# Kernel tuning notes

Hardware: AMD Instinct MI355X
Metric: run time of the kernel (lower is better)

## Reference

```python
import jax, jax.numpy as jnp
import numpy as np

N_NODES = 50000
N_EDGES = 800000
EPS = 1e-16

def _gat_layer(x, row, col, W, a_src, a_dst, b, heads, concat):
    N = x.shape[0]
    C = a_src.shape[1]
    h = (x @ W).reshape(N, heads, C)                       # [N,H,C]
    al_src = jnp.sum(h * a_src, axis=-1)                    # [N,H]
    al_dst = jnp.sum(h * a_dst, axis=-1)                    # [N,H]
    e = jax.nn.leaky_relu(al_src[row] + al_dst[col], 0.2)   # [E,H]
    # segment softmax over destination node (col)
    m = jax.ops.segment_max(e, col, num_segments=N)
    e = jnp.exp(e - m[col])
    s = jax.ops.segment_sum(e, col, num_segments=N)
    alpha = e / (s[col] + EPS)                              # [E,H]
    msg = h[row] * alpha[:, :, None]                        # [E,H,C]
    out = jax.ops.segment_sum(msg, col, num_segments=N)     # [N,H,C]
    out = out.reshape(N, heads * C) if concat else out.mean(axis=1)
    return out + b

def setup_inputs() -> dict:
    key = jax.random.key(0)
    ks = jax.random.split(key, 16)
    d_in, hid, d_out, d_edge, H = 64, 64, 32, 16, 4
    inp = {
        "x": jax.random.normal(ks[0], (N_NODES, d_in), jnp.float32),
        "edge_index": jax.random.randint(ks[1], (2, N_EDGES), 0, N_NODES, jnp.int32),
        "edge_attr": jax.random.normal(ks[2], (N_EDGES, d_edge), jnp.float32),
        "W1": jax.random.normal(ks[3], (d_in, H * hid), jnp.float32) * 0.1,
        "a1_src": jax.random.normal(ks[4], (H, hid), jnp.float32) * 0.1,
        "a1_dst": jax.random.normal(ks[5], (H, hid), jnp.float32) * 0.1,
        "b1": jax.random.normal(ks[6], (H * hid,), jnp.float32) * 0.1,
        "W2": jax.random.normal(ks[7], (H * hid, hid), jnp.float32) * 0.05,
        "a2_src": jax.random.normal(ks[8], (1, hid), jnp.float32) * 0.1,
        "a2_dst": jax.random.normal(ks[9], (1, hid), jnp.float32) * 0.1,
        "b2": jax.random.normal(ks[10], (hid,), jnp.float32) * 0.1,
        "Wn": jax.random.normal(ks[11], (hid, d_out), jnp.float32) * 0.1,
        "bn": jax.random.normal(ks[12], (d_out,), jnp.float32) * 0.1,
        "We": jax.random.normal(ks[13], (2 * hid + d_edge, 1), jnp.float32) * 0.1,
        "be": jax.random.normal(ks[14], (1,), jnp.float32) * 0.1,
    }
    return inp

def reference(x, edge_index, edge_attr, W1, a1_src, a1_dst, b1, W2, a2_src, a2_dst, b2, Wn, bn, We, be):
    N = x.shape[0]
    row0, col0 = edge_index[0], edge_index[1]
    # PyG GATConv default: add self loops for message passing
    loops = jnp.arange(N, dtype=edge_index.dtype)
    row = jnp.concatenate([row0, loops])
    col = jnp.concatenate([col0, loops])
    h = jax.nn.elu(_gat_layer(x, row, col, W1, a1_src, a1_dst, b1, heads=4, concat=True))
    h = jax.nn.elu(_gat_layer(h, row, col, W2, a2_src, a2_dst, b2, heads=1, concat=False))
    node_out = h @ Wn + bn                                   # [N, out]
    edge_feat = jnp.concatenate([h[row0], h[col0], edge_attr], axis=1)  # [E, 2*hid+d_edge]
    edge_out = edge_feat @ We + be                           # [E, 1]
    return (node_out, edge_out)
```

## Files before the change

kernel.cpp:

```cpp
#include <hip/hip_runtime.h>
#include <hip/hip_bf16.h>

#define N_NODES 50000
#define N_EDGES 800000
#define N_TOT   850000
#define MAXD    128

#define NBUCK 196
#define BCAP  8192

typedef __hip_bfloat16 bf16;
typedef __attribute__((ext_vector_type(8))) short bf16x8;
typedef __attribute__((ext_vector_type(4))) float f32x4;

__device__ __forceinline__ unsigned short f2bu(float v){
  union { bf16 b; unsigned short u; } cv; cv.b = __float2bfloat16(v); return cv.u;
}
__device__ __forceinline__ float bflo(unsigned int d){ return __uint_as_float(d << 16); }
__device__ __forceinline__ float bfhi(unsigned int d){ return __uint_as_float(d & 0xffff0000u); }

__global__ __launch_bounds__(256) void initb_kernel(int* __restrict__ bcur){
  int i = threadIdx.x;
  if (i < NBUCK) bcur[i] = i * BCAP;
}

__global__ __launch_bounds__(256) void binscatter_kernel(const int* __restrict__ ei,
    int* __restrict__ bcur, unsigned int* __restrict__ pairbuf){
  __shared__ int hist[NBUCK];
  __shared__ int gbase[NBUCK];
  int tid = threadIdx.x;
  if (tid < NBUCK) hist[tid] = 0;
  __syncthreads();
  int base = blockIdx.x * 4096;
  #pragma unroll 4
  for (int i = 0; i < 16; ++i) {
    int k = base + i*256 + tid;
    if (k < N_TOT) {
      int c = (k < N_EDGES) ? ei[N_EDGES + k] : (k - N_EDGES);
      atomicAdd(&hist[c >> 8], 1);
    }
  }
  __syncthreads();
  if (tid < NBUCK) {
    int h = hist[tid];
    gbase[tid] = h ? atomicAdd(&bcur[tid], h) : 0;
    hist[tid] = 0;
  }
  __syncthreads();
  #pragma unroll 4
  for (int i = 0; i < 16; ++i) {
    int k = base + i*256 + tid;
    if (k < N_TOT) {
      int r, c;
      if (k < N_EDGES) { r = ei[k]; c = ei[N_EDGES + k]; } else { r = c = k - N_EDGES; }
      int b = c >> 8;
      int lpos = atomicAdd(&hist[b], 1);
      pairbuf[gbase[b] + lpos] = (unsigned)r | ((unsigned)(c & 255) << 16);
    }
  }
}

__global__ __launch_bounds__(256) void bcount_kernel(const unsigned int* __restrict__ pairbuf,
    const int* __restrict__ bcur, int* __restrict__ cnt){
  __shared__ int lhist[256];
  int b = blockIdx.x, tid = threadIdx.x;
  lhist[tid] = 0;
  __syncthreads();
  int base = b * BCAP;
  int size = bcur[b] - base; if (size > BCAP) size = BCAP;
  for (int j = tid; j < size; j += 256)
    atomicAdd(&lhist[pairbuf[base + j] >> 16], 1);
  __syncthreads();
  int node = b*256 + tid;
  if (node < N_NODES) cnt[node] = lhist[tid];
}

__global__ __launch_bounds__(1024) void scanA_kernel(const int* __restrict__ cnt, int* __restrict__ psum){
  __shared__ int wsum[16];
  int tid = threadIdx.x, i = blockIdx.x*1024 + tid;
  int v = (i < N_NODES) ? cnt[i] : 0;
  #pragma unroll
  for (int off = 32; off; off >>= 1) v += __shfl_xor(v, off, 64);
  if ((tid & 63) == 0) wsum[tid >> 6] = v;
  __syncthreads();
  if (tid < 64) {
    int t = (tid < 16) ? wsum[tid] : 0;
    #pragma unroll
    for (int off = 8; off; off >>= 1) t += __shfl_xor(t, off, 64);
    if (tid == 0) psum[blockIdx.x] = t;
  }
}

__global__ __launch_bounds__(64) void scanB_kernel(int* __restrict__ psum, int nparts){
  int lane = threadIdx.x;
  int v = (lane < nparts) ? psum[lane] : 0;
  #pragma unroll
  for (int off = 1; off < 64; off <<= 1) {
    int t = __shfl_up(v, off, 64);
    if (lane >= off) v += t;
  }
  int e = __shfl_up(v, 1, 64);
  if (lane == 0) e = 0;
  if (lane < nparts) psum[lane] = e;
}

__global__ __launch_bounds__(1024) void scanC_kernel(const int* __restrict__ cnt, const int* __restrict__ psum,
                                                     int* __restrict__ offs){
  __shared__ int sm[1024];
  int tid = threadIdx.x, b = blockIdx.x, i = b*1024 + tid;
  int v = (i < N_NODES) ? cnt[i] : 0;
  sm[tid] = v;
  __syncthreads();
  for (int off = 1; off < 1024; off <<= 1) {
    int t = (tid >= off) ? sm[tid - off] : 0;
    __syncthreads();
    sm[tid] += t;
    __syncthreads();
  }
  if (i < N_NODES) offs[i] = psum[b] + sm[tid] - v;
  if (b == 0 && tid == 0) offs[N_NODES] = N_TOT;
}

__global__ __launch_bounds__(256) void lscatter_kernel(const unsigned int* __restrict__ pairbuf,
    const int* __restrict__ bcur, const int* __restrict__ offs, int* __restrict__ srcs){
  __shared__ int lcur[256];
  int b = blockIdx.x, tid = threadIdx.x;
  int lo = b*256;
  if (lo + tid < N_NODES) lcur[tid] = offs[lo + tid];
  __syncthreads();
  int base = b * BCAP;
  int size = bcur[b] - base; if (size > BCAP) size = BCAP;
  for (int j = tid; j < size; j += 256) {
    unsigned v = pairbuf[base + j];
    int pos = atomicAdd(&lcur[v >> 16], 1);
    srcs[pos] = (int)(v & 0xFFFFu);
  }
}

__global__ __launch_bounds__(256) void wfrag_kernel(const float* __restrict__ W1, const float* __restrict__ W2,
    const float* __restrict__ a1s, const float* __restrict__ a1d,
    unsigned short* __restrict__ wf1, unsigned short* __restrict__ wf2,
    float* __restrict__ ws1, float* __restrict__ wd1){
  int b = blockIdx.x, tid = threadIdx.x;
  if (b < 128) {
    int i = b*256 + tid;
    if (i < 16384) {
      int k = i >> 8, n = i & 255;
      int kk = k >> 5, qq = (k >> 3) & 3, j = k & 7, nt = n >> 4, cc = n & 15;
      wf1[(((kk*16 + nt)*4 + qq)*16 + cc)*8 + j] = f2bu(W1[i]);
    } else {
      int i2 = i - 16384;
      int k = i2 >> 6, n = i2 & 63;
      int kk = k >> 5, qq = (k >> 3) & 3, j = k & 7, ch = n >> 4, cc = n & 15;
      wf2[(((kk*4 + ch)*4 + qq)*16 + cc)*8 + j] = f2bu(W2[i2]);
    }
  } else {
    int k = tid >> 2, h = tid & 3;
    const float* wrow = W1 + k*256 + h*64;
    const float* as = a1s + h*64;
    const float* ad = a1d + h*64;
    float ss = 0.f, sd = 0.f;
    #pragma unroll 8
    for (int c = 0; c < 64; ++c) {
      float wv = wrow[c];
      ss = fmaf(wv, as[c], ss);
      sd = fmaf(wv, ad[c], sd);
    }
    ws1[k*4 + h] = ss;
    wd1[k*4 + h] = sd;
  }
}

__global__ __launch_bounds__(256) void xprep_kernel(const float* __restrict__ x,
    const float* __restrict__ ws1, const float* __restrict__ wd1,
    unsigned short* __restrict__ xb, float* __restrict__ al1s, float* __restrict__ al1d){
  __shared__ float sws[64][4], swd[64][4];
  int tid = threadIdx.x;
  sws[tid >> 2][tid & 3] = ws1[tid];
  swd[tid >> 2][tid & 3] = wd1[tid];
  __syncthreads();
  int lane = tid & 63, wave = tid >> 6;
  int g = lane & 15, sub = lane >> 4;
  int n = blockIdx.x*16 + wave*4 + sub;
  float4 xv = *(const float4*)(x + (size_t)n*64 + g*4);
  uint2 dd;
  dd.x = (unsigned)f2bu(xv.x) | ((unsigned)f2bu(xv.y) << 16);
  dd.y = (unsigned)f2bu(xv.z) | ((unsigned)f2bu(xv.w) << 16);
  ((uint2*)xb)[(size_t)n*16 + g] = dd;
  int c0 = g*4;
  float ps0 = 0.f, ps1 = 0.f, ps2 = 0.f, ps3 = 0.f;
  float pd0 = 0.f, pd1 = 0.f, pd2 = 0.f, pd3 = 0.f;
  float xc[4] = {xv.x, xv.y, xv.z, xv.w};
  #pragma unroll
  for (int i = 0; i < 4; ++i) {
    int c = c0 + i;
    ps0 = fmaf(xc[i], sws[c][0], ps0); ps1 = fmaf(xc[i], sws[c][1], ps1);
    ps2 = fmaf(xc[i], sws[c][2], ps2); ps3 = fmaf(xc[i], sws[c][3], ps3);
    pd0 = fmaf(xc[i], swd[c][0], pd0); pd1 = fmaf(xc[i], swd[c][1], pd1);
    pd2 = fmaf(xc[i], swd[c][2], pd2); pd3 = fmaf(xc[i], swd[c][3], pd3);
  }
  #pragma unroll
  for (int off = 1; off < 16; off <<= 1) {
    ps0 += __shfl_xor(ps0, off, 64); ps1 += __shfl_xor(ps1, off, 64);
    ps2 += __shfl_xor(ps2, off, 64); ps3 += __shfl_xor(ps3, off, 64);
    pd0 += __shfl_xor(pd0, off, 64); pd1 += __shfl_xor(pd1, off, 64);
    pd2 += __shfl_xor(pd2, off, 64); pd3 += __shfl_xor(pd3, off, 64);
  }
  if (g < 4)      al1s[(size_t)n*4 + g]       = (g==0)?ps0:(g==1)?ps1:(g==2)?ps2:ps3;
  else if (g < 8) al1d[(size_t)n*4 + (g-4)]   = (g==4)?pd0:(g==5)?pd1:(g==6)?pd2:pd3;
}

__global__ __launch_bounds__(256, 8) void attn1x_kernel(const unsigned short* __restrict__ xb,
    const float* __restrict__ al1s, const float* __restrict__ al1d,
    const int* __restrict__ offs, const int* __restrict__ srcs,
    bf16* __restrict__ ag){
  __shared__ __align__(16) float ebuf[4][MAXD+4][4];
  __shared__ int sbuf[4][MAXD+4];

  int wave = threadIdx.x >> 6, lane = threadIdx.x & 63;
  int n = blockIdx.x*4 + wave;
  int start = offs[n], end = offs[n+1];
  int deg = end - start;
  int lim = deg < MAXD ? deg : MAXD;
  float4 aldv = *(const float4*)(al1d + (size_t)n*4);
  float ald0 = aldv.x, ald1 = aldv.y, ald2 = aldv.z, ald3 = aldv.w;

  float s0 = 0.f, s1 = 0.f, s2 = 0.f, s3 = 0.f;
  {
    int idx = lane;
    for (int j = start + lane; j < end; j += 64, idx += 64) {
      int r = srcs[j];
      float4 als = *(const float4*)(al1s + (size_t)r*4);
      float e0 = als.x + ald0; e0 = e0 >= 0.f ? e0 : 0.2f*e0; float p0 = __expf(e0); s0 += p0;
      float e1 = als.y + ald1; e1 = e1 >= 0.f ? e1 : 0.2f*e1; float p1 = __expf(e1); s1 += p1;
      float e2 = als.z + ald2; e2 = e2 >= 0.f ? e2 : 0.2f*e2; float p2 = __expf(e2); s2 += p2;
      float e3 = als.w + ald3; e3 = e3 >= 0.f ? e3 : 0.2f*e3; float p3 = __expf(e3); s3 += p3;
      if (idx < MAXD) {
        sbuf[wave][idx] = r;
        *(float4*)&ebuf[wave][idx][0] = make_float4(p0, p1, p2, p3);
      }
    }
  }
  if (lane < 4) {
    int ip = lim + lane;
    sbuf[wave][ip] = 0;
    *(float4*)&ebuf[wave][ip][0] = make_float4(0.f, 0.f, 0.f, 0.f);
  }
  #pragma unroll
  for (int off = 32; off; off >>= 1) {
    s0 += __shfl_xor(s0, off, 64);
    s1 += __shfl_xor(s1, off, 64);
    s2 += __shfl_xor(s2, off, 64);
    s3 += __shfl_xor(s3, off, 64);
  }
  float inv0 = 1.f/(s0 + 1e-16f), inv1 = 1.f/(s1 + 1e-16f);
  float inv2 = 1.f/(s2 + 1e-16f), inv3 = 1.f/(s3 + 1e-16f);

  int cl = lane & 15, es = lane >> 4;
  float acc[4][4];
  #pragma unroll
  for (int h = 0; h < 4; ++h)
    #pragma unroll
    for (int i = 0; i < 4; ++i) acc[h][i] = 0.f;
  {
    const uint2* base2 = (const uint2*)xb;
    #pragma unroll 2
    for (int jj = 0; jj < lim; jj += 4) {
      int idx = jj + es;
      int r = sbuf[wave][idx];
      float4 pv = *(const float4*)&ebuf[wave][idx][0];
      uint2 d = base2[(size_t)r*16 + cl];
      float c0 = bflo(d.x), c1 = bfhi(d.x), c2 = bflo(d.y), c3 = bfhi(d.y);
      acc[0][0] = fmaf(pv.x, c0, acc[0][0]); acc[0][1] = fmaf(pv.x, c1, acc[0][1]);
      acc[0][2] = fmaf(pv.x, c2, acc[0][2]); acc[0][3] = fmaf(pv.x, c3, acc[0][3]);
      acc[1][0] = fmaf(pv.y, c0, acc[1][0]); acc[1][1] = fmaf(pv.y, c1, acc[1][1]);
      acc[1][2] = fmaf(pv.y, c2, acc[1][2]); acc[1][3] = fmaf(pv.y, c3, acc[1][3]);
      acc[2][0] = fmaf(pv.z, c0, acc[2][0]); acc[2][1] = fmaf(pv.z, c1, acc[2][1]);
      acc[2][2] = fmaf(pv.z, c2, acc[2][2]); acc[2][3] = fmaf(pv.z, c3, acc[2][3]);
      acc[3][0] = fmaf(pv.w, c0, acc[3][0]); acc[3][1] = fmaf(pv.w, c1, acc[3][1]);
      acc[3][2] = fmaf(pv.w, c2, acc[3][2]); acc[3][3] = fmaf(pv.w, c3, acc[3][3]);
    }
  }
  if (deg > MAXD) {
    const uint2* base2 = (const uint2*)xb;
    for (int jj = MAXD; jj < deg; jj += 4) {
      int idx = jj + es;
      bool ok = idx < deg;
      int j = ok ? (start + idx) : start;
      int r = srcs[j];
      float4 als = *(const float4*)(al1s + (size_t)r*4);
      float e0 = als.x + ald0; e0 = e0 >= 0.f ? e0 : 0.2f*e0; float p0 = __expf(e0);
      float e1 = als.y + ald1; e1 = e1 >= 0.f ? e1 : 0.2f*e1; float p1 = __expf(e1);
      float e2 = als.z + ald2; e2 = e2 >= 0.f ? e2 : 0.2f*e2; float p2 = __expf(e2);
      float e3 = als.w + ald3; e3 = e3 >= 0.f ? e3 : 0.2f*e3; float p3 = __expf(e3);
      float m = ok ? 1.f : 0.f;
      uint2 d = base2[(size_t)r*16 + cl];
      float c0 = bflo(d.x)*m, c1 = bfhi(d.x)*m, c2 = bflo(d.y)*m, c3 = bfhi(d.y)*m;
      acc[0][0] = fmaf(p0, c0, acc[0][0]); acc[0][1] = fmaf(p0, c1, acc[0][1]);
      acc[0][2] = fmaf(p0, c2, acc[0][2]); acc[0][3] = fmaf(p0, c3, acc[0][3]);
      acc[1][0] = fmaf(p1, c0, acc[1][0]); acc[1][1] = fmaf(p1, c1, acc[1][1]);
      acc[1][2] = fmaf(p1, c2, acc[1][2]); acc[1][3] = fmaf(p1, c3, acc[1][3]);
      acc[2][0] = fmaf(p2, c0, acc[2][0]); acc[2][1] = fmaf(p2, c1, acc[2][1]);
      acc[2][2] = fmaf(p2, c2, acc[2][2]); acc[2][3] = fmaf(p2, c3, acc[2][3]);
      acc[3][0] = fmaf(p3, c0, acc[3][0]); acc[3][1] = fmaf(p3, c1, acc[3][1]);
      acc[3][2] = fmaf(p3, c2, acc[3][2]); acc[3][3] = fmaf(p3, c3, acc[3][3]);
    }
  }
  #pragma unroll
  for (int h = 0; h < 4; ++h)
    #pragma unroll
    for (int i = 0; i < 4; ++i) {
      acc[h][i] += __shfl_xor(acc[h][i], 16, 64);
      acc[h][i] += __shfl_xor(acc[h][i], 32, 64);
    }
  {
    float invh = (es==0)?inv0:(es==1)?inv1:(es==2)?inv2:inv3;
    float o0 = ((es==0)?acc[0][0]:(es==1)?acc[1][0]:(es==2)?acc[2][0]:acc[3][0]) * invh;
    float o1 = ((es==0)?acc[0][1]:(es==1)?acc[1][1]:(es==2)?acc[2][1]:acc[3][1]) * invh;
    float o2 = ((es==0)?acc[0][2]:(es==1)?acc[1][2]:(es==2)?acc[2][2]:acc[3][2]) * invh;
    float o3 = ((es==0)?acc[0][3]:(es==1)?acc[1][3]:(es==2)?acc[2][3]:acc[3][3]) * invh;
    uint2 dd;
    dd.x = (unsigned)f2bu(o0) | ((unsigned)f2bu(o1) << 16);
    dd.y = (unsigned)f2bu(o2) | ((unsigned)f2bu(o3) << 16);
    ((uint2*)ag)[(size_t)n*64 + lane] = dd;
  }
}

__global__ __launch_bounds__(256) void gemm1b_kernel(const unsigned short* __restrict__ ag,
    const unsigned short* __restrict__ wf1, const float* __restrict__ b1, bf16* __restrict__ h1){
  __shared__ __align__(16) unsigned short ctile[32*264];
  int tid = threadIdx.x, wave = tid >> 6, lane = tid & 63;
  int q = lane >> 4, c = lane & 15;
  int n0 = blockIdx.x * 64;

  union { uint4 u; bf16x8 v; } bfr[2][4];
  #pragma unroll
  for (int kk = 0; kk < 2; ++kk)
    #pragma unroll
    for (int nti = 0; nti < 4; ++nti)
      bfr[kk][nti].u = *(const uint4*)(wf1 + (size_t)((((kk*16 + wave*4 + nti)*4 + q)*16 + c)*8));

  float b1v[4];
  #pragma unroll
  for (int nti = 0; nti < 4; ++nti) b1v[nti] = b1[(wave*4 + nti)*16 + c];

  #pragma unroll
  for (int half = 0; half < 2; ++half) {
    #pragma unroll
    for (int sti = 0; sti < 2; ++sti) {
      int st = half*2 + sti;
      int row = n0 + st*16 + c;
      if (row >= N_NODES) row = N_NODES - 1;
      bf16x8 afr[2];
      #pragma unroll
      for (int kk = 0; kk < 2; ++kk) {
        union { uint4 u; bf16x8 v; } a;
        a.u = *(const uint4*)(ag + (size_t)row*256 + wave*64 + kk*32 + q*8);
        afr[kk] = a.v;
      }
      #pragma unroll
      for (int nti = 0; nti < 4; ++nti) {
        f32x4 acc = {0.f, 0.f, 0.f, 0.f};
        #pragma unroll
        for (int kk = 0; kk < 2; ++kk)
          acc = __builtin_amdgcn_mfma_f32_16x16x32_bf16(afr[kk], bfr[kk][nti].v, acc, 0, 0, 0);
        int lrow = sti*16 + q*4, nt = wave*4 + nti;
        #pragma unroll
        for (int r = 0; r < 4; ++r) {
          float o = acc[r] + b1v[nti];
          o = o > 0.f ? o : expm1f(o);
          ctile[(lrow + r)*264 + nt*16 + c] = f2bu(o);
        }
      }
    }
    __syncthreads();
    #pragma unroll 1
    for (int i = 0; i < 8; ++i) {
      int lr = wave*8 + i;
      int node = n0 + half*32 + lr;
      if (node < N_NODES) {
        uint2 dd = *(const uint2*)&ctile[lr*264 + lane*4];
        ((uint2*)h1)[(size_t)node*64 + lane] = dd;
      }
    }
    __syncthreads();
  }
}

__global__ __launch_bounds__(256) void gemm2_kernel(const bf16* __restrict__ h1, const unsigned short* __restrict__ wf2,
    const float* __restrict__ a2s, const float* __restrict__ a2d,
    bf16* __restrict__ h2pre, float* __restrict__ al2s, float* __restrict__ al2d){
  __shared__ __align__(16) float ctile[64][65];
  int tid = threadIdx.x, wave = tid >> 6, lane = tid & 63;
  int q = lane >> 4, c = lane & 15;
  int n0 = blockIdx.x * 64;

  union { uint4 u; bf16x8 v; } bfr[8];
  #pragma unroll
  for (int kk = 0; kk < 8; ++kk)
    bfr[kk].u = *(const uint4*)(wf2 + (size_t)((((kk*4 + wave)*4 + q)*16 + c)*8));

  const unsigned short* h1u = (const unsigned short*)h1;
  #pragma unroll 1
  for (int st = 0; st < 4; ++st) {
    if (n0 + st*16 >= N_NODES) break;
    f32x4 acc = {0.f, 0.f, 0.f, 0.f};
    size_t arow = (size_t)(n0 + st*16 + c)*256 + q*8;
    #pragma unroll
    for (int kk = 0; kk < 8; ++kk) {
      union { uint4 u; bf16x8 v; } a;
      a.u = *(const uint4*)(h1u + arow + kk*32);
      acc = __builtin_amdgcn_mfma_f32_16x16x32_bf16(a.v, bfr[kk].v, acc, 0, 0, 0);
    }
    #pragma unroll
    for (int r = 0; r < 4; ++r)
      ctile[st*16 + q*4 + r][wave*16 + c] = acc[r];
  }
  __syncthreads();

  float as = a2s[lane], ad = a2d[lane];
  #pragma unroll 1
  for (int i = 0; i < 16; ++i) {
    int node = n0 + wave*16 + i;
    if (node >= N_NODES) break;
    float val = ctile[wave*16 + i][lane];
    ((unsigned short*)h2pre)[(size_t)node*64 + lane] = f2bu(val);
    float ps = val*as, pd = val*ad;
    #pragma unroll
    for (int off = 32; off; off >>= 1) { ps += __shfl_xor(ps, off, 64); pd += __shfl_xor(pd, off, 64); }
    if (lane == 0) { al2s[node] = ps; al2d[node] = pd; }
  }
}

__global__ __launch_bounds__(512, 8) void attn2_kernel(const bf16* __restrict__ h2pre,
    const float* __restrict__ al2s, const float* __restrict__ al2d,
    const int* __restrict__ offs, const int* __restrict__ srcs,
    const float* __restrict__ b2, float* __restrict__ h2f){
  __shared__ float ebuf[8][MAXD+8];
  __shared__ int   sbuf[8][MAXD+8];
  int wave = threadIdx.x >> 6, lane = threadIdx.x & 63;
  int n = blockIdx.x*8 + wave;
  int start = offs[n], end = offs[n+1];
  int deg = end - start;
  int lim = deg < MAXD ? deg : MAXD;
  float ald = al2d[n];

  float sm = 0.f;
  {
    int idx = lane;
    for (int j = start + lane; j < end; j += 64, idx += 64) {
      int r = srcs[j];
      float t = al2s[r] + ald; t = t >= 0.f ? t : 0.2f*t;
      float p = __expf(t); sm += p;
      if (idx < MAXD) { sbuf[wave][idx] = r; ebuf[wave][idx] = p; }
    }
  }
  if (lane < 8) { int ip = lim + lane; sbuf[wave][ip] = 0; ebuf[wave][ip] = 0.f; }
  #pragma unroll
  for (int off = 32; off; off >>= 1) sm += __shfl_xor(sm, off, 64);
  float inv = 1.f/(sm + 1e-16f);

  int cl = lane & 7, es = lane >> 3;
  float acc0 = 0.f, acc1 = 0.f, acc2 = 0.f, acc3 = 0.f;
  float acc4 = 0.f, acc5 = 0.f, acc6 = 0.f, acc7 = 0.f;
  {
    const uint4* base4 = (const uint4*)h2pre;
    #pragma unroll 2
    for (int jj = 0; jj < lim; jj += 8) {
      int idx = jj + es;
      int r = sbuf[wave][idx];
      float p = ebuf[wave][idx];
      uint4 d = base4[(size_t)r*8 + cl];
      acc0 = fmaf(p, bflo(d.x), acc0);
      acc1 = fmaf(p, bfhi(d.x), acc1);
      acc2 = fmaf(p, bflo(d.y), acc2);
      acc3 = fmaf(p, bfhi(d.y), acc3);
      acc4 = fmaf(p, bflo(d.z), acc4);
      acc5 = fmaf(p, bfhi(d.z), acc5);
      acc6 = fmaf(p, bflo(d.w), acc6);
      acc7 = fmaf(p, bfhi(d.w), acc7);
    }
  }
  if (deg > MAXD) {
    const uint4* base4 = (const uint4*)h2pre;
    for (int jj = MAXD; jj < deg; jj += 8) {
      int idx = jj + es;
      bool ok = idx < deg;
      int j = ok ? (start + idx) : start;
      int r = srcs[j];
      float t = al2s[r] + ald; t = t >= 0.f ? t : 0.2f*t;
      float p = ok ? __expf(t) : 0.f;
      uint4 d = base4[(size_t)r*8 + cl];
      acc0 = fmaf(p, bflo(d.x), acc0);
      acc1 = fmaf(p, bfhi(d.x), acc1);
      acc2 = fmaf(p, bflo(d.y), acc2);
      acc3 = fmaf(p, bfhi(d.y), acc3);
      acc4 = fmaf(p, bflo(d.z), acc4);
      acc5 = fmaf(p, bfhi(d.z), acc5);
      acc6 = fmaf(p, bflo(d.w), acc6);
      acc7 = fmaf(p, bfhi(d.w), acc7);
    }
  }
  #pragma unroll
  for (int off = 8; off < 64; off <<= 1) {
    acc0 += __shfl_xor(acc0, off, 64);
    acc1 += __shfl_xor(acc1, off, 64);
    acc2 += __shfl_xor(acc2, off, 64);
    acc3 += __shfl_xor(acc3, off, 64);
    acc4 += __shfl_xor(acc4, off, 64);
    acc5 += __shfl_xor(acc5, off, 64);
    acc6 += __shfl_xor(acc6, off, 64);
    acc7 += __shfl_xor(acc7, off, 64);
  }

  if (es == 0) {
    float4 b2a = *(const float4*)(b2 + cl*8);
    float4 b2b = *(const float4*)(b2 + cl*8 + 4);
    float o0 = acc0*inv + b2a.x; o0 = o0 > 0.f ? o0 : expm1f(o0);
    float o1 = acc1*inv + b2a.y; o1 = o1 > 0.f ? o1 : expm1f(o1);
    float o2 = acc2*inv + b2a.z; o2 = o2 > 0.f ? o2 : expm1f(o2);
    float o3 = acc3*inv + b2a.w; o3 = o3 > 0.f ? o3 : expm1f(o3);
    float o4 = acc4*inv + b2b.x; o4 = o4 > 0.f ? o4 : expm1f(o4);
    float o5 = acc5*inv + b2b.y; o5 = o5 > 0.f ? o5 : expm1f(o5);
    float o6 = acc6*inv + b2b.z; o6 = o6 > 0.f ? o6 : expm1f(o6);
    float o7 = acc7*inv + b2b.w; o7 = o7 > 0.f ? o7 : expm1f(o7);
    *(float4*)(h2f + (size_t)n*64 + cl*8)     = make_float4(o0, o1, o2, o3);
    *(float4*)(h2f + (size_t)n*64 + cl*8 + 4) = make_float4(o4, o5, o6, o7);
  }
}

__global__ __launch_bounds__(256) void head_kernel(const float* __restrict__ h2f,
    const float* __restrict__ Wn, const float* __restrict__ bn, const float* __restrict__ We,
    float* __restrict__ u, float* __restrict__ v, float* __restrict__ node_out){
  __shared__ __align__(16) float sh[8][64];
  int tid = threadIdx.x;
  int nb = blockIdx.x*8;
  {
    float2 t = *(const float2*)(h2f + (size_t)nb*64 + tid*2);
    *(float2*)&sh[tid >> 5][(tid & 31)*2] = t;
  }
  __syncthreads();
  int wave = tid >> 6, lane = tid & 63;
  int sub = lane >> 5, j = lane & 31;
  int local = wave*2 + sub;
  int n = nb + local;
  const float* h = sh[local];
  float a = 0.f;
  #pragma unroll 16
  for (int k = 0; k < 64; ++k)
    a = fmaf(h[k], Wn[k*32 + j], a);
  node_out[(size_t)n*32 + j] = a + bn[j];
  float pu = h[j]*We[j] + h[j+32]*We[j+32];
  float pv = h[j]*We[64+j] + h[j+32]*We[96+j];
  #pragma unroll
  for (int off = 1; off < 32; off <<= 1) {
    pu += __shfl_xor(pu, off, 64);
    pv += __shfl_xor(pv, off, 64);
  }
  if (j == 0) { u[n] = pu; v[n] = pv; }
}

__global__ __launch_bounds__(256) void edge_kernel(const int* __restrict__ ei, const float* __restrict__ ea,
    const float* __restrict__ u, const float* __restrict__ v,
    const float* __restrict__ We, const float* __restrict__ be, float* __restrict__ out){
  int k = blockIdx.x*256 + threadIdx.x;
  int r = ei[k], c = ei[N_EDGES + k];
  float val = u[r] + v[c] + be[0];
  const float4* wp = (const float4*)(We + 128);
  const float4* p  = (const float4*)(ea + (size_t)k*16);
  #pragma unroll
  for (int jj = 0; jj < 4; jj++) {
    float4 q = p[jj], wq = wp[jj];
    val = fmaf(q.x, wq.x, val);
    val = fmaf(q.y, wq.y, val);
    val = fmaf(q.z, wq.z, val);
    val = fmaf(q.w, wq.w, val);
  }
  out[k] = val;
}

extern "C" void kernel_launch(void* const* d_in, const int* in_sizes, int n_in,
                              void* d_out, int out_size, void* d_ws, size_t ws_size,
                              hipStream_t stream) {
  const float* x   = (const float*)d_in[0];
  const int*   ei  = (const int*)d_in[1];
  const float* ea  = (const float*)d_in[2];
  const float* W1  = (const float*)d_in[3];
  const float* a1s = (const float*)d_in[4];
  const float* a1d = (const float*)d_in[5];
  const float* b1  = (const float*)d_in[6];
  const float* W2  = (const float*)d_in[7];
  const float* a2s = (const float*)d_in[8];
  const float* a2d = (const float*)d_in[9];
  const float* b2  = (const float*)d_in[10];
  const float* Wn  = (const float*)d_in[11];
  const float* bn  = (const float*)d_in[12];
  const float* We  = (const float*)d_in[13];
  const float* be  = (const float*)d_in[14];
  float* out = (float*)d_out;

  char* w = (char*)d_ws;
  int*   offs   = (int*)(w);
  int*   cnt    = (int*)(w + 200016);
  int*   bcur   = (int*)(w + 400016);
  int*   srcs   = (int*)(w + 600016);
  float* al1s   = (float*)(w + 4000016);
  float* al1d   = (float*)(w + 4800016);
  float* al2s   = (float*)(w + 5600016);
  float* al2d   = (float*)(w + 5800016);
  float* uu     = (float*)(w + 6000016);
  float* vv     = (float*)(w + 6200016);
  bf16*  h2pre  = (bf16*)(w + 6400016);
  bf16*  ag     = (bf16*)(w + 12800016);
  int*   psum   = (int*)(w + 38400016);
  bf16*  h1     = (bf16*)(w + 38400224);
  unsigned short* wf1 = (unsigned short*)cnt;
  float* ws1 = (float*)(w + 232784);
  float* wd1 = (float*)(w + 233808);
  unsigned short* wf2 = (unsigned short*)bcur;
  unsigned short* xb  = (unsigned short*)h2pre;
  unsigned int* pairbuf = (unsigned int*)h1;
  float* h2f = (float*)ag;

  const int NPART = (N_NODES + 1023) / 1024;

  initb_kernel     <<<1, 256, 0, stream>>>(bcur);
  binscatter_kernel<<<(N_TOT + 4095)/4096, 256, 0, stream>>>(ei, bcur, pairbuf);
  bcount_kernel    <<<NBUCK, 256, 0, stream>>>(pairbuf, bcur, cnt);
  scanA_kernel     <<<NPART, 1024, 0, stream>>>(cnt, psum);
  scanB_kernel     <<<1, 64, 0, stream>>>(psum, NPART);
  scanC_kernel     <<<NPART, 1024, 0, stream>>>(cnt, psum, offs);
  lscatter_kernel  <<<NBUCK, 256, 0, stream>>>(pairbuf, bcur, offs, srcs);
  wfrag_kernel     <<<129, 256, 0, stream>>>(W1, W2, a1s, a1d, wf1, wf2, ws1, wd1);
  xprep_kernel     <<<N_NODES/16, 256, 0, stream>>>(x, ws1, wd1, xb, al1s, al1d);
  attn1x_kernel    <<<N_NODES/4, 256, 0, stream>>>(xb, al1s, al1d, offs, srcs, ag);
  gemm1b_kernel    <<<(N_NODES + 63)/64, 256, 0, stream>>>((const unsigned short*)ag, wf1, b1, h1);
  gemm2_kernel     <<<(N_NODES + 63)/64, 256, 0, stream>>>(h1, wf2, a2s, a2d, h2pre, al2s, al2d);
  attn2_kernel     <<<N_NODES/8, 512, 0, stream>>>(h2pre, al2s, al2d, offs, srcs, b2, h2f);
  head_kernel      <<<N_NODES/8, 256, 0, stream>>>(h2f, Wn, bn, We, uu, vv, out);
  edge_kernel      <<<N_EDGES/256, 256, 0, stream>>>(ei, ea, uu, vv, We, be, out + (size_t)N_NODES*32);
}
```

Measured before the change: 323.4 us.

## Merge CSR-build kernels and fuse output head into second attention kernel

The CSR construction drops the separate count, three-pass node scan and scatter kernels. It uses a tiny 196-bucket scan plus a per-bucket kernel that builds a local histogram, scans it, writes offsets and scatters sources. Bucket-cursor init is folded into the weight-prep kernel. The node head (Wn projection plus the u/v edge projections) now runs inside attn2 via lane shuffles, which removes the h2f round trip and one launch. This cuts several small launches and global traffic, at the cost of serial shared-memory scans inside each bucket block.

```diff
diff --git a/kernel.cpp b/kernel.cpp
--- a/kernel.cpp
+++ b/kernel.cpp
@@ -19,128 +19,10 @@
 __device__ __forceinline__ float bflo(unsigned int d){ return __uint_as_float(d << 16); }
 __device__ __forceinline__ float bfhi(unsigned int d){ return __uint_as_float(d & 0xffff0000u); }
 
-__global__ __launch_bounds__(256) void initb_kernel(int* __restrict__ bcur){
-  int i = threadIdx.x;
-  if (i < NBUCK) bcur[i] = i * BCAP;
-}
-
-__global__ __launch_bounds__(256) void binscatter_kernel(const int* __restrict__ ei,
-    int* __restrict__ bcur, unsigned int* __restrict__ pairbuf){
-  __shared__ int hist[NBUCK];
-  __shared__ int gbase[NBUCK];
-  int tid = threadIdx.x;
-  if (tid < NBUCK) hist[tid] = 0;
-  __syncthreads();
-  int base = blockIdx.x * 4096;
-  #pragma unroll 4
-  for (int i = 0; i < 16; ++i) {
-    int k = base + i*256 + tid;
-    if (k < N_TOT) {
-      int c = (k < N_EDGES) ? ei[N_EDGES + k] : (k - N_EDGES);
-      atomicAdd(&hist[c >> 8], 1);
-    }
-  }
-  __syncthreads();
-  if (tid < NBUCK) {
-    int h = hist[tid];
-    gbase[tid] = h ? atomicAdd(&bcur[tid], h) : 0;
-    hist[tid] = 0;
-  }
-  __syncthreads();
-  #pragma unroll 4
-  for (int i = 0; i < 16; ++i) {
-    int k = base + i*256 + tid;
-    if (k < N_TOT) {
-      int r, c;
-      if (k < N_EDGES) { r = ei[k]; c = ei[N_EDGES + k]; } else { r = c = k - N_EDGES; }
-      int b = c >> 8;
-      int lpos = atomicAdd(&hist[b], 1);
-      pairbuf[gbase[b] + lpos] = (unsigned)r | ((unsigned)(c & 255) << 16);
-    }
-  }
-}
-
-__global__ __launch_bounds__(256) void bcount_kernel(const unsigned int* __restrict__ pairbuf,
-    const int* __restrict__ bcur, int* __restrict__ cnt){
-  __shared__ int lhist[256];
-  int b = blockIdx.x, tid = threadIdx.x;
-  lhist[tid] = 0;
-  __syncthreads();
-  int base = b * BCAP;
-  int size = bcur[b] - base; if (size > BCAP) size = BCAP;
-  for (int j = tid; j < size; j += 256)
-    atomicAdd(&lhist[pairbuf[base + j] >> 16], 1);
-  __syncthreads();
-  int node = b*256 + tid;
-  if (node < N_NODES) cnt[node] = lhist[tid];
-}
-
-__global__ __launch_bounds__(1024) void scanA_kernel(const int* __restrict__ cnt, int* __restrict__ psum){
-  __shared__ int wsum[16];
-  int tid = threadIdx.x, i = blockIdx.x*1024 + tid;
-  int v = (i < N_NODES) ? cnt[i] : 0;
-  #pragma unroll
-  for (int off = 32; off; off >>= 1) v += __shfl_xor(v, off, 64);
-  if ((tid & 63) == 0) wsum[tid >> 6] = v;
-  __syncthreads();
-  if (tid < 64) {
-    int t = (tid < 16) ? wsum[tid] : 0;
-    #pragma unroll
-    for (int off = 8; off; off >>= 1) t += __shfl_xor(t, off, 64);
-    if (tid == 0) psum[blockIdx.x] = t;
-  }
-}
-
-__global__ __launch_bounds__(64) void scanB_kernel(int* __restrict__ psum, int nparts){
-  int lane = threadIdx.x;
-  int v = (lane < nparts) ? psum[lane] : 0;
-  #pragma unroll
-  for (int off = 1; off < 64; off <<= 1) {
-    int t = __shfl_up(v, off, 64);
-    if (lane >= off) v += t;
-  }
-  int e = __shfl_up(v, 1, 64);
-  if (lane == 0) e = 0;
-  if (lane < nparts) psum[lane] = e;
-}
-
-__global__ __launch_bounds__(1024) void scanC_kernel(const int* __restrict__ cnt, const int* __restrict__ psum,
-                                                     int* __restrict__ offs){
-  __shared__ int sm[1024];
-  int tid = threadIdx.x, b = blockIdx.x, i = b*1024 + tid;
-  int v = (i < N_NODES) ? cnt[i] : 0;
-  sm[tid] = v;
-  __syncthreads();
-  for (int off = 1; off < 1024; off <<= 1) {
-    int t = (tid >= off) ? sm[tid - off] : 0;
-    __syncthreads();
-    sm[tid] += t;
-    __syncthreads();
-  }
-  if (i < N_NODES) offs[i] = psum[b] + sm[tid] - v;
-  if (b == 0 && tid == 0) offs[N_NODES] = N_TOT;
-}
-
-__global__ __launch_bounds__(256) void lscatter_kernel(const unsigned int* __restrict__ pairbuf,
-    const int* __restrict__ bcur, const int* __restrict__ offs, int* __restrict__ srcs){
-  __shared__ int lcur[256];
-  int b = blockIdx.x, tid = threadIdx.x;
-  int lo = b*256;
-  if (lo + tid < N_NODES) lcur[tid] = offs[lo + tid];
-  __syncthreads();
-  int base = b * BCAP;
-  int size = bcur[b] - base; if (size > BCAP) size = BCAP;
-  for (int j = tid; j < size; j += 256) {
-    unsigned v = pairbuf[base + j];
-    int pos = atomicAdd(&lcur[v >> 16], 1);
-    srcs[pos] = (int)(v & 0xFFFFu);
-  }
-}
-
 __global__ __launch_bounds__(256) void wfrag_kernel(const float* __restrict__ W1, const float* __restrict__ W2,
     const float* __restrict__ a1s, const float* __restrict__ a1d,
     unsigned short* __restrict__ wf1, unsigned short* __restrict__ wf2,
-    float* __restrict__ ws1, float* __restrict__ wd1){
+    float* __restrict__ ws1, float* __restrict__ wd1, int* __restrict__ bcur){
   int b = blockIdx.x, tid = threadIdx.x;
   if (b < 128) {
     int i = b*256 + tid;
@@ -154,7 +36,7 @@
       int kk = k >> 5, qq = (k >> 3) & 3, j = k & 7, ch = n >> 4, cc = n & 15;
       wf2[(((kk*4 + ch)*4 + qq)*16 + cc)*8 + j] = f2bu(W2[i2]);
     }
-  } else {
+  } else if (b == 128) {
     int k = tid >> 2, h = tid & 3;
     const float* wrow = W1 + k*256 + h*64;
     const float* as = a1s + h*64;
@@ -168,6 +50,101 @@
     }
     ws1[k*4 + h] = ss;
     wd1[k*4 + h] = sd;
+  } else {
+    if (tid < NBUCK) bcur[tid] = tid * BCAP;
+  }
+}
+
+__global__ __launch_bounds__(256) void binscatter_kernel(const int* __restrict__ ei,
+    int* __restrict__ bcur, unsigned int* __restrict__ pairbuf){
+  __shared__ int hist[NBUCK];
+  __shared__ int gbase[NBUCK];
+  int tid = threadIdx.x;
+  if (tid < NBUCK) hist[tid] = 0;
+  __syncthreads();
+  int base = blockIdx.x * 4096;
+  #pragma unroll 4
+  for (int i = 0; i < 16; ++i) {
+    int k = base + i*256 + tid;
+    if (k < N_TOT) {
+      int c = (k < N_EDGES) ? ei[N_EDGES + k] : (k - N_EDGES);
+      atomicAdd(&hist[c >> 8], 1);
+    }
+  }
+  __syncthreads();
+  if (tid < NBUCK) {
+    int h = hist[tid];
+    gbase[tid] = h ? atomicAdd(&bcur[tid], h) : 0;
+    hist[tid] = 0;
+  }
+  __syncthreads();
+  #pragma unroll 4
+  for (int i = 0; i < 16; ++i) {
+    int k = base + i*256 + tid;
+    if (k < N_TOT) {
+      int r, c;
+      if (k < N_EDGES) { r = ei[k]; c = ei[N_EDGES + k]; } else { r = c = k - N_EDGES; }
+      int b = c >> 8;
+      int lpos = atomicAdd(&hist[b], 1);
+      pairbuf[gbase[b] + lpos] = (unsigned)r | ((unsigned)(c & 255) << 16);
+    }
+  }
+}
+
+__global__ __launch_bounds__(256) void scan196_kernel(const int* __restrict__ bcur,
+    int* __restrict__ bbase, int* __restrict__ offs){
+  __shared__ int sm[256];
+  int tid = threadIdx.x;
+  int v = 0;
+  if (tid < NBUCK) {
+    v = bcur[tid] - tid*BCAP;
+    if (v < 0) v = 0; if (v > BCAP) v = BCAP;
+  }
+  sm[tid] = v;
+  __syncthreads();
+  for (int off = 1; off < 256; off <<= 1) {
+    int t = (tid >= off) ? sm[tid - off] : 0;
+    __syncthreads();
+    sm[tid] += t;
+    __syncthreads();
+  }
+  if (tid < NBUCK) bbase[tid] = sm[tid] - v;
+  if (tid == 0) offs[N_NODES] = N_TOT;
+}
+
+__global__ __launch_bounds__(256) void lscatter2_kernel(const unsigned int* __restrict__ pairbuf,
+    const int* __restrict__ bcur, const int* __restrict__ bbase,
+    int* __restrict__ offs, int* __restrict__ srcs){
+  __shared__ int lhist[256];
+  __shared__ int lcur[256];
+  int b = blockIdx.x, tid = threadIdx.x;
+  lhist[tid] = 0;
+  __syncthreads();
+  int base = b * BCAP;
+  int size = bcur[b] - base; if (size > BCAP) size = BCAP; if (size < 0) size = 0;
+  for (int j = tid; j < size; j += 256)
+    atomicAdd(&lhist[pairbuf[base + j] >> 16], 1);
+  __syncthreads();
+  int v = lhist[tid];
+  lcur[tid] = v;
+  __syncthreads();
+  for (int off = 1; off < 256; off <<= 1) {
+    int t = (tid >= off) ? lcur[tid - off] : 0;
+    __syncthreads();
+    lcur[tid] += t;
+    __syncthreads();
+  }
+  int excl = lcur[tid] - v;
+  int gpos = bbase[b] + excl;
+  int node = b*256 + tid;
+  if (node < N_NODES) offs[node] = gpos;
+  __syncthreads();
+  lcur[tid] = gpos;
+  __syncthreads();
+  for (int j = tid; j < size; j += 256) {
+    unsigned pv = pairbuf[base + j];
+    int pos = atomicAdd(&lcur[pv >> 16], 1);
+    srcs[pos] = (int)(pv & 0xFFFFu);
   }
 }
 
@@ -435,7 +412,9 @@
 __global__ __launch_bounds__(512, 8) void attn2_kernel(const bf16* __restrict__ h2pre,
     const float* __restrict__ al2s, const float* __restrict__ al2d,
     const int* __restrict__ offs, const int* __restrict__ srcs,
-    const float* __restrict__ b2, float* __restrict__ h2f){
+    const float* __restrict__ b2, const float* __restrict__ Wn, const float* __restrict__ bn,
+    const float* __restrict__ We,
+    float* __restrict__ u, float* __restrict__ v, float* __restrict__ node_out){
   __shared__ float ebuf[8][MAXD+8];
   __shared__ int   sbuf[8][MAXD+8];
   int wave = threadIdx.x >> 6, lane = threadIdx.x & 63;
@@ -513,51 +492,59 @@
     acc7 += __shfl_xor(acc7, off, 64);
   }
 
-  if (es == 0) {
-    float4 b2a = *(const float4*)(b2 + cl*8);
-    float4 b2b = *(const float4*)(b2 + cl*8 + 4);
-    float o0 = acc0*inv + b2a.x; o0 = o0 > 0.f ? o0 : expm1f(o0);
-    float o1 = acc1*inv + b2a.y; o1 = o1 > 0.f ? o1 : expm1f(o1);
-    float o2 = acc2*inv + b2a.z; o2 = o2 > 0.f ? o2 : expm1f(o2);
-    float o3 = acc3*inv + b2a.w; o3 = o3 > 0.f ? o3 : expm1f(o3);
-    float o4 = acc4*inv + b2b.x; o4 = o4 > 0.f ? o4 : expm1f(o4);
-    float o5 = acc5*inv + b2b.y; o5 = o5 > 0.f ? o5 : expm1f(o5);
-    float o6 = acc6*inv + b2b.z; o6 = o6 > 0.f ? o6 : expm1f(o6);
-    float o7 = acc7*inv + b2b.w; o7 = o7 > 0.f ? o7 : expm1f(o7);
-    *(float4*)(h2f + (size_t)n*64 + cl*8)     = make_float4(o0, o1, o2, o3);
-    *(float4*)(h2f + (size_t)n*64 + cl*8 + 4) = make_float4(o4, o5, o6, o7);
-  }
-}
-
-__global__ __launch_bounds__(256) void head_kernel(const float* __restrict__ h2f,
-    const float* __restrict__ Wn, const float* __restrict__ bn, const float* __restrict__ We,
-    float* __restrict__ u, float* __restrict__ v, float* __restrict__ node_out){
-  __shared__ __align__(16) float sh[8][64];
-  int tid = threadIdx.x;
-  int nb = blockIdx.x*8;
+  float4 b2a = *(const float4*)(b2 + cl*8);
+  float4 b2b = *(const float4*)(b2 + cl*8 + 4);
+  float ov[8];
+  ov[0] = acc0*inv + b2a.x; ov[0] = ov[0] > 0.f ? ov[0] : expm1f(ov[0]);
+  ov[1] = acc1*inv + b2a.y; ov[1] = ov[1] > 0.f ? ov[1] : expm1f(ov[1]);
+  ov[2] = acc2*inv + b2a.z; ov[2] = ov[2] > 0.f ? ov[2] : expm1f(ov[2]);
+  ov[3] = acc3*inv + b2a.w; ov[3] = ov[3] > 0.f ? ov[3] : expm1f(ov[3]);
+  ov[4] = acc4*inv + b2b.x; ov[4] = ov[4] > 0.f ? ov[4] : expm1f(ov[4]);
+  ov[5] = acc5*inv + b2b.y; ov[5] = ov[5] > 0.f ? ov[5] : expm1f(ov[5]);
+  ov[6] = acc6*inv + b2b.z; ov[6] = ov[6] > 0.f ? ov[6] : expm1f(ov[6]);
+  ov[7] = acc7*inv + b2b.w; ov[7] = ov[7] > 0.f ? ov[7] : expm1f(ov[7]);
+
   {
-    float2 t = *(const float2*)(h2f + (size_t)nb*64 + tid*2);
-    *(float2*)&sh[tid >> 5][(tid & 31)*2] = t;
-  }
-  __syncthreads();
-  int wave = tid >> 6, lane = tid & 63;
-  int sub = lane >> 5, j = lane & 31;
-  int local = wave*2 + sub;
-  int n = nb + local;
-  const float* h = sh[local];
-  float a = 0.f;
-  #pragma unroll 16
-  for (int k = 0; k < 64; ++k)
-    a = fmaf(h[k], Wn[k*32 + j], a);
-  node_out[(size_t)n*32 + j] = a + bn[j];
-  float pu = h[j]*We[j] + h[j+32]*We[j+32];
-  float pv = h[j]*We[64+j] + h[j+32]*We[96+j];
-  #pragma unroll
-  for (int off = 1; off < 32; off <<= 1) {
-    pu += __shfl_xor(pu, off, 64);
-    pv += __shfl_xor(pv, off, 64);
-  }
-  if (j == 0) { u[n] = pu; v[n] = pv; }
+    int c0 = cl*8;
+    float p0 = 0.f, p1 = 0.f, p2 = 0.f, p3 = 0.f;
+    #pragma unroll
+    for (int i = 0; i < 8; ++i) {
+      float4 wr = *(const float4*)(Wn + (size_t)(c0 + i)*32 + es*4);
+      p0 = fmaf(ov[i], wr.x, p0);
+      p1 = fmaf(ov[i], wr.y, p1);
+      p2 = fmaf(ov[i], wr.z, p2);
+      p3 = fmaf(ov[i], wr.w, p3);
+    }
+    #pragma unroll
+    for (int off = 1; off < 8; off <<= 1) {
+      p0 += __shfl_xor(p0, off, 64);
+      p1 += __shfl_xor(p1, off, 64);
+      p2 += __shfl_xor(p2, off, 64);
+      p3 += __shfl_xor(p3, off, 64);
+    }
+    if (cl < 4) {
+      float pr = (cl==0)?p0:(cl==1)?p1:(cl==2)?p2:p3;
+      int j = es*4 + cl;
+      node_out[(size_t)n*32 + j] = pr + bn[j];
+    }
+  }
+  {
+    int c0 = cl*8;
+    float4 wea = *(const float4*)(We + c0);
+    float4 web = *(const float4*)(We + c0 + 4);
+    float4 wva = *(const float4*)(We + 64 + c0);
+    float4 wvb = *(const float4*)(We + 64 + c0 + 4);
+    float pu = ov[0]*wea.x + ov[1]*wea.y + ov[2]*wea.z + ov[3]*wea.w
+             + ov[4]*web.x + ov[5]*web.y + ov[6]*web.z + ov[7]*web.w;
+    float pv = ov[0]*wva.x + ov[1]*wva.y + ov[2]*wva.z + ov[3]*wva.w
+             + ov[4]*wvb.x + ov[5]*wvb.y + ov[6]*wvb.z + ov[7]*wvb.w;
+    #pragma unroll
+    for (int off = 1; off < 8; off <<= 1) {
+      pu += __shfl_xor(pu, off, 64);
+      pv += __shfl_xor(pv, off, 64);
+    }
+    if (lane == 0) { u[n] = pu; v[n] = pv; }
+  }
 }
 
 __global__ __launch_bounds__(256) void edge_kernel(const int* __restrict__ ei, const float* __restrict__ ea,
@@ -601,8 +588,12 @@
 
   char* w = (char*)d_ws;
   int*   offs   = (int*)(w);
-  int*   cnt    = (int*)(w + 200016);
+  unsigned short* wf1 = (unsigned short*)(w + 200016);
+  float* ws1    = (float*)(w + 232784);
+  float* wd1    = (float*)(w + 233808);
+  unsigned short* wf2 = (unsigned short*)(w + 234832);
   int*   bcur   = (int*)(w + 400016);
+  int*   bbase  = (int*)(w + 400816);
   int*   srcs   = (int*)(w + 600016);
   float* al1s   = (float*)(w + 4000016);
   float* al1d   = (float*)(w + 4800016);
@@ -612,31 +603,19 @@
   float* vv     = (float*)(w + 6200016);
   bf16*  h2pre  = (bf16*)(w + 6400016);
   bf16*  ag     = (bf16*)(w + 12800016);
-  int*   psum   = (int*)(w + 38400016);
   bf16*  h1     = (bf16*)(w + 38400224);
-  unsigned short* wf1 = (unsigned short*)cnt;
-  float* ws1 = (float*)(w + 232784);
-  float* wd1 = (float*)(w + 233808);
-  unsigned short* wf2 = (unsigned short*)bcur;
   unsigned short* xb  = (unsigned short*)h2pre;
   unsigned int* pairbuf = (unsigned int*)h1;
-  float* h2f = (float*)ag;
-
-  const int NPART = (N_NODES + 1023) / 1024;
-
-  initb_kernel     <<<1, 256, 0, stream>>>(bcur);
+
+  wfrag_kernel     <<<130, 256, 0, stream>>>(W1, W2, a1s, a1d, wf1, wf2, ws1, wd1, bcur);
   binscatter_kernel<<<(N_TOT + 4095)/4096, 256, 0, stream>>>(ei, bcur, pairbuf);
-  bcount_kernel    <<<NBUCK, 256, 0, stream>>>(pairbuf, bcur, cnt);
-  scanA_kernel     <<<NPART, 1024, 0, stream>>>(cnt, psum);
-  scanB_kernel     <<<1, 64, 0, stream>>>(psum, NPART);
-  scanC_kernel     <<<NPART, 1024, 0, stream>>>(cnt, psum, offs);
-  lscatter_kernel  <<<NBUCK, 256, 0, stream>>>(pairbuf, bcur, offs, srcs);
-  wfrag_kernel     <<<129, 256, 0, stream>>>(W1, W2, a1s, a1d, wf1, wf2, ws1, wd1);
+  scan196_kernel   <<<1, 256, 0, stream>>>(bcur, bbase, offs);
+  lscatter2_kernel <<<NBUCK, 256, 0, stream>>>(pairbuf, bcur, bbase, offs, srcs);
   xprep_kernel     <<<N_NODES/16, 256, 0, stream>>>(x, ws1, wd1, xb, al1s, al1d);
   attn1x_kernel    <<<N_NODES/4, 256, 0, stream>>>(xb, al1s, al1d, offs, srcs, ag);
   gemm1b_kernel    <<<(N_NODES + 63)/64, 256, 0, stream>>>((const unsigned short*)ag, wf1, b1, h1);
   gemm2_kernel     <<<(N_NODES + 63)/64, 256, 0, stream>>>(h1, wf2, a2s, a2d, h2pre, al2s, al2d);
-  attn2_kernel     <<<N_NODES/8, 512, 0, stream>>>(h2pre, al2s, al2d, offs, srcs, b2, h2f);
-  head_kernel      <<<N_NODES/8, 256, 0, stream>>>(h2f, Wn, bn, We, uu, vv, out);
+  attn2_kernel     <<<N_NODES/8, 512, 0, stream>>>(h2pre, al2s, al2d, offs, srcs, b2, Wn, bn, We,
+                                                   uu, vv, out);
   edge_kernel      <<<N_EDGES/256, 256, 0, stream>>>(ei, ea, uu, vv, We, be, out + (size_t)N_NODES*32);
 }
```

Result: slower. 338.5 us (+4.6%).
